# Optimization experiments

Hardware: AMD Instinct MI355X
Metric: run time of the kernel (lower is better)

## Reference

```python
import jax, jax.numpy as jnp
import numpy as np
import math

HEAD = 4
D_MODEL = 128
N_NODES = 2048
SEQ_LEN = 1
D_K = D_MODEL // HEAD
BATCH = 64


def conv1x1_relu(x, w, b):
    # x: [B, C, N, L], w: [O, C], b: [O]  (1x1 Conv2d + ReLU; dropout is identity in eval)
    return jax.nn.relu(jnp.einsum('oc,bcnl->bonl', w, x) + b[None, :, None, None])


def setup_inputs() -> dict:
    key = jax.random.key(0)
    ks = jax.random.split(key, 12)
    s = 0.05
    return {
        'x': jax.random.normal(ks[0], (BATCH, D_MODEL, N_NODES, SEQ_LEN), jnp.float32),
        'q_w': jax.random.normal(ks[1], (D_MODEL, D_MODEL), jnp.float32) * s,
        'q_b': jnp.zeros((D_MODEL,), jnp.float32),
        'v_w': jax.random.normal(ks[2], (D_MODEL, D_MODEL), jnp.float32) * s,
        'v_b': jnp.zeros((D_MODEL,), jnp.float32),
        'c_w': jax.random.normal(ks[3], (D_MODEL, D_MODEL), jnp.float32) * s,
        'c_b': jnp.zeros((D_MODEL,), jnp.float32),
        'memory': jax.random.normal(ks[4], (HEAD, SEQ_LEN, N_NODES, D_K), jnp.float32) * s,
        'nodevec1': jax.random.normal(ks[5], (N_NODES, 10), jnp.float32),
        'nodevec2': jax.random.normal(ks[6], (10, N_NODES), jnp.float32),
        'weights_pool': jax.random.normal(ks[7], (SEQ_LEN, 3, 3), jnp.float32) * s,
        'bias_pool': jax.random.normal(ks[8], (N_NODES, D_K), jnp.float32) * s,
        'aff_w': jnp.ones((D_MODEL, N_NODES, SEQ_LEN), jnp.float32),
        'aff_b': jnp.zeros((D_MODEL, N_NODES, SEQ_LEN), jnp.float32),
    }


def reference(x, q_w, q_b, v_w, v_b, c_w, c_b, memory, nodevec1, nodevec2,
              weights_pool, bias_pool, aff_w, aff_b):
    B = x.shape[0]
    scale = math.sqrt(D_K)

    query = conv1x1_relu(x, q_w, q_b)
    value = conv1x1_relu(x, v_w, v_b)

    # [B, d_model, N, L] -> [B, h, d_k, N, L] -> [B, h, L, N, d_k]
    def split_heads(t):
        return t.reshape(B, HEAD, D_K, N_NODES, SEQ_LEN).transpose(0, 1, 4, 3, 2)

    query = split_heads(query)
    value = split_heads(value)

    key_ = jax.nn.softmax(memory / scale, axis=-1)      # [h, L, N, d_k]
    query = jax.nn.softmax(query / scale, axis=-1)      # [B, h, L, N, d_k]

    Aapt = jax.nn.softmax(jax.nn.relu(nodevec1 @ nodevec2), axis=-1)  # [N, N]

    kv = jnp.einsum('hlnx,bhlny->bhlxy', key_, value)          # [B,h,L,d_k,d_k]
    attn_qkv = jnp.einsum('bhlnx,bhlxy->bhlny', query, kv)     # [B,h,L,N,d_k]

    weights = jnp.einsum('nm,dio->nio', Aapt, weights_pool)    # [N,3,3]
    bias_dyn = Aapt @ bias_pool                                # [N,d_k]
    attn_dyn = jnp.einsum('bhlnc,nio->bhlnc', value, weights) + bias_dyn[None, None, None, :, :]

    out = attn_qkv + attn_dyn                                  # [B,h,L,N,d_k]
    out = out.transpose(0, 1, 4, 3, 2).reshape(B, D_MODEL, N_NODES, SEQ_LEN)
    out = conv1x1_relu(out, c_w, c_b)

    # num_nodes (2048) not in [170, 358, 5] -> affine-residual branch runs
    out = out * aff_w[None] + aff_b[None] + out
    return out
```

## Files before the change

kernel.cpp:

```cpp
#include <hip/hip_runtime.h>

#define NB 64
#define CH 128
#define NNODE 2048
#define NH 4
#define DKK 32
#define INVS 0.17677669529663687f

typedef __bf16 bf16x8 __attribute__((ext_vector_type(8)));
typedef float f32x4 __attribute__((ext_vector_type(4)));
typedef unsigned short ushort_t;

union U16x8 { uint4 u; bf16x8 b; unsigned short s[8]; };
union U16x4 { uint2 u; unsigned short s[4]; };

__device__ inline bf16x8 as_bf16x8(uint4 u){ U16x8 x; x.u = u; return x.b; }
__device__ inline unsigned short f2b(float f){ __bf16 h = (__bf16)f; return __builtin_bit_cast(unsigned short, h); }
__device__ inline float b2f(unsigned short u){ __bf16 h = __builtin_bit_cast(__bf16, u); return (float)h; }

__global__ __launch_bounds__(256) void k0_prep(const float* __restrict__ qw,
    const float* __restrict__ vw, const float* __restrict__ cw,
    const float* __restrict__ memory, const float* __restrict__ bias_pool,
    ushort_t* __restrict__ wqb, ushort_t* __restrict__ wvb, ushort_t* __restrict__ wcb,
    ushort_t* __restrict__ keysT, float* __restrict__ bias_dyn,
    ushort_t* __restrict__ bpT)
{
  int gid = blockIdx.x * 256 + threadIdx.x;
  if (gid < 16384) { wqb[gid] = f2b(qw[gid]); wvb[gid] = f2b(vw[gid]); wcb[gid] = f2b(cw[gid]); }
  bias_dyn[gid] = 0.f;
  { int k = gid >> 11, m = gid & 2047;
    bpT[gid] = f2b(bias_pool[m * 32 + k]); }
  if (gid < 8192) {
    int h = gid >> 11, n = gid & 2047;
    const float* src = memory + (size_t)gid * 32;
    float v[32]; float m = -1e30f;
    #pragma unroll
    for (int i = 0; i < 32; ++i) { v[i] = src[i] * INVS; m = fmaxf(m, v[i]); }
    float s = 0.f;
    #pragma unroll
    for (int i = 0; i < 32; ++i) { v[i] = __expf(v[i] - m); s += v[i]; }
    float inv = 1.f / s;
    #pragma unroll
    for (int i = 0; i < 32; ++i)
      keysT[(size_t)(h * 32 + i) * 2048 + n] = f2b(v[i] * inv);
  }
}

__global__ __launch_bounds__(256) void kb1(const float* __restrict__ nv1,
    const float* __restrict__ nv2, ushort_t* __restrict__ Ebuf)
{
  int n = blockIdx.x; int tid = threadIdx.x;
  float a1[10];
  #pragma unroll
  for (int d = 0; d < 10; ++d) a1[d] = nv1[n * 10 + d];
  int m0 = tid * 8;
  float s[8];
  #pragma unroll
  for (int j = 0; j < 8; ++j) s[j] = 0.f;
  #pragma unroll
  for (int d = 0; d < 10; ++d) {
    const float* p = nv2 + d * 2048 + m0;
    float4 u = *(const float4*)p; float4 v = *(const float4*)(p + 4);
    s[0] += a1[d] * u.x; s[1] += a1[d] * u.y; s[2] += a1[d] * u.z; s[3] += a1[d] * u.w;
    s[4] += a1[d] * v.x; s[5] += a1[d] * v.y; s[6] += a1[d] * v.z; s[7] += a1[d] * v.w;
  }
  float e[8]; float sum = 0.f;
  #pragma unroll
  for (int j = 0; j < 8; ++j) { e[j] = __expf(fmaxf(s[j], 0.f)); sum += e[j]; }
  #pragma unroll
  for (int d = 1; d < 64; d <<= 1) sum += __shfl_xor(sum, d);
  __shared__ float red[4];
  if ((tid & 63) == 0) red[tid >> 6] = sum;
  __syncthreads();
  float inv = 1.f / (red[0] + red[1] + red[2] + red[3]);
  U16x8 o;
  #pragma unroll
  for (int j = 0; j < 8; ++j) o.s[j] = f2b(e[j] * inv);
  *(uint4*)(Ebuf + (size_t)n * 2048 + m0) = o.u;
}

__global__ __launch_bounds__(256) void kb2(const ushort_t* __restrict__ Ebuf,
    const ushort_t* __restrict__ bpT, float* __restrict__ bias_dyn)
{
  int bid = blockIdx.x;
  int n0 = (bid >> 3) * 128;
  int m0 = (bid & 7) * 256;
  int tid = threadIdx.x; int wv = tid >> 6; int lane = tid & 63;
  int quad = lane >> 4; int l16 = lane & 15;
  int r0 = n0 + 32 * wv;
  f32x4 zero4 = {0.f,0.f,0.f,0.f};
  f32x4 acc[2][2];
  acc[0][0] = zero4; acc[0][1] = zero4; acc[1][0] = zero4; acc[1][1] = zero4;
  for (int ks = 0; ks < 256; ks += 32) {
    int mb = m0 + ks + 8 * quad;
    bf16x8 a0 = *(const bf16x8*)(Ebuf + (size_t)(r0 + l16) * 2048 + mb);
    bf16x8 a1 = *(const bf16x8*)(Ebuf + (size_t)(r0 + 16 + l16) * 2048 + mb);
    bf16x8 b0 = *(const bf16x8*)(bpT + (size_t)l16 * 2048 + mb);
    bf16x8 b1 = *(const bf16x8*)(bpT + (size_t)(16 + l16) * 2048 + mb);
    acc[0][0] = __builtin_amdgcn_mfma_f32_16x16x32_bf16(a0, b0, acc[0][0], 0, 0, 0);
    acc[0][1] = __builtin_amdgcn_mfma_f32_16x16x32_bf16(a0, b1, acc[0][1], 0, 0, 0);
    acc[1][0] = __builtin_amdgcn_mfma_f32_16x16x32_bf16(a1, b0, acc[1][0], 0, 0, 0);
    acc[1][1] = __builtin_amdgcn_mfma_f32_16x16x32_bf16(a1, b1, acc[1][1], 0, 0, 0);
  }
  #pragma unroll
  for (int rt = 0; rt < 2; ++rt)
    #pragma unroll
    for (int ct = 0; ct < 2; ++ct)
      #pragma unroll
      for (int r = 0; r < 4; ++r)
        atomicAdd(bias_dyn + (size_t)(r0 + 16*rt + 4*quad + r) * 32 + 16*ct + l16,
                  acc[rt][ct][r]);
}

__global__ __launch_bounds__(256) void k1_qv(const float* __restrict__ x,
    const ushort_t* __restrict__ wqb, const ushort_t* __restrict__ wvb,
    const float* __restrict__ qbias, const float* __restrict__ vbias,
    ushort_t* __restrict__ QsT, ushort_t* __restrict__ VT)
{
  int bid = blockIdx.x; int b = bid >> 5; int n0 = (bid & 31) * 64;
  int tid = threadIdx.x; int wv = tid >> 6; int lane = tid & 63;
  int quad = lane >> 4; int l16 = lane & 15;
  __shared__ __align__(16) ushort_t XT[64][136];
  __shared__ __align__(16) ushort_t QO[64][136];

  uint4 wq[2][4], wvv[2][4];
  #pragma unroll
  for (int ct = 0; ct < 2; ++ct)
    #pragma unroll
    for (int k0 = 0; k0 < 4; ++k0) {
      int off = (32 * wv + 16 * ct + l16) * 128 + 32 * k0 + 8 * quad;
      wq[ct][k0]  = *(const uint4*)(wqb + off);
      wvv[ct][k0] = *(const uint4*)(wvb + off);
    }
  float4 qb4[2], vb4[2];
  #pragma unroll
  for (int ct = 0; ct < 2; ++ct) {
    qb4[ct] = *(const float4*)(qbias + 32 * wv + 16 * ct + 4 * quad);
    vb4[ct] = *(const float4*)(vbias + 32 * wv + 16 * ct + 4 * quad);
  }

  #pragma unroll
  for (int p = 0; p < 2; ++p) {
    int c4 = 4 * ((tid >> 4) + 16 * p);
    int n4 = 4 * (tid & 15);
    float4 r[4];
    #pragma unroll
    for (int j = 0; j < 4; ++j)
      r[j] = *(const float4*)(x + (size_t)(b * 128 + c4 + j) * 2048 + n0 + n4);
    #pragma unroll
    for (int i = 0; i < 4; ++i) {
      U16x4 w;
      w.s[0] = f2b(((const float*)&r[0])[i]);
      w.s[1] = f2b(((const float*)&r[1])[i]);
      w.s[2] = f2b(((const float*)&r[2])[i]);
      w.s[3] = f2b(((const float*)&r[3])[i]);
      *(uint2*)&XT[n4 + i][c4] = w.u;
    }
  }
  __syncthreads();

  f32x4 zero4 = {0.f,0.f,0.f,0.f};
  f32x4 av[4][2];

  #pragma unroll
  for (int nt = 0; nt < 4; ++nt) {
    f32x4 aq[2]; aq[0] = zero4; aq[1] = zero4;
    f32x4 avv[2]; avv[0] = zero4; avv[1] = zero4;
    #pragma unroll
    for (int k0 = 0; k0 < 4; ++k0) {
      bf16x8 bfrag = *(const bf16x8*)&XT[16 * nt + l16][32 * k0 + 8 * quad];
      #pragma unroll
      for (int ct = 0; ct < 2; ++ct) {
        aq[ct]  = __builtin_amdgcn_mfma_f32_16x16x32_bf16(as_bf16x8(wq[ct][k0]),  bfrag, aq[ct],  0, 0, 0);
        avv[ct] = __builtin_amdgcn_mfma_f32_16x16x32_bf16(as_bf16x8(wvv[ct][k0]), bfrag, avv[ct], 0, 0, 0);
      }
    }
    float sq[2][4]; float mx = -1e30f;
    #pragma unroll
    for (int ct = 0; ct < 2; ++ct)
      #pragma unroll
      for (int r = 0; r < 4; ++r) {
        sq[ct][r] = fmaxf(aq[ct][r] + ((const float*)&qb4[ct])[r], 0.f) * INVS;
        mx = fmaxf(mx, sq[ct][r]);
      }
    mx = fmaxf(mx, __shfl_xor(mx, 16));
    mx = fmaxf(mx, __shfl_xor(mx, 32));
    float sum = 0.f;
    #pragma unroll
    for (int ct = 0; ct < 2; ++ct)
      #pragma unroll
      for (int r = 0; r < 4; ++r) { sq[ct][r] = __expf(sq[ct][r] - mx); sum += sq[ct][r]; }
    sum += __shfl_xor(sum, 16);
    sum += __shfl_xor(sum, 32);
    float inv = 1.f / sum;
    #pragma unroll
    for (int ct = 0; ct < 2; ++ct) {
      U16x4 w;
      #pragma unroll
      for (int r = 0; r < 4; ++r) w.s[r] = f2b(sq[ct][r] * inv);
      *(uint2*)&QO[16 * nt + l16][32 * wv + 16 * ct + 4 * quad] = w.u;
    }
    av[nt][0] = avv[0]; av[nt][1] = avv[1];
  }
  __syncthreads();

  #pragma unroll
  for (int nt = 0; nt < 4; ++nt)
    #pragma unroll
    for (int ct = 0; ct < 2; ++ct) {
      U16x4 w;
      #pragma unroll
      for (int r = 0; r < 4; ++r)
        w.s[r] = f2b(fmaxf(av[nt][ct][r] + ((const float*)&vb4[ct])[r], 0.f));
      *(uint2*)&XT[16 * nt + l16][32 * wv + 16 * ct + 4 * quad] = w.u;
    }
  __syncthreads();

  #pragma unroll
  for (int j = 0; j < 4; ++j) {
    int id = tid + 256 * j; int n = id >> 4; int u = id & 15;
    size_t go = (size_t)(b * 2048 + n0 + n) * 128 + 8 * u;
    *(uint4*)(QsT + go) = *(uint4*)&QO[n][8 * u];
    *(uint4*)(VT  + go) = *(uint4*)&XT[n][8 * u];
  }
}

__global__ __launch_bounds__(256) void k2_kv(const ushort_t* __restrict__ keysT,
    const ushort_t* __restrict__ VT, float* __restrict__ kvp)
{
  int bid = blockIdx.x; int b = bid >> 3; int nb = (bid & 7) * 256;
  int tid = threadIdx.x; int wv = tid >> 6; int lane = tid & 63;
  int quad = lane >> 4; int l16 = lane & 15;
  __shared__ __align__(16) ushort_t Vraw[128][136];

  f32x4 zero4 = {0.f,0.f,0.f,0.f};
  f32x4 acc[2][2];
  acc[0][0] = zero4; acc[0][1] = zero4; acc[1][0] = zero4; acc[1][1] = zero4;

  for (int chunk = 0; chunk < 2; ++chunk) {
    int nc = nb + 128 * chunk;
    if (chunk) __syncthreads();
    #pragma unroll
    for (int p = 0; p < 8; ++p) {
      int id = tid + 256 * p; int n = id >> 4; int g = id & 15;
      *(uint4*)&Vraw[n][8 * g] = *(const uint4*)(VT + (size_t)(b * 2048 + nc + n) * 128 + 8 * g);
    }
    __syncthreads();
    const ushort_t* kT = keysT + (size_t)(wv * 32) * 2048 + nc;
    #pragma unroll
    for (int ks = 0; ks < 4; ++ks) {
      int k0 = 32 * ks + 8 * quad;
      bf16x8 a0 = *(const bf16x8*)(kT + (size_t)l16 * 2048 + k0);
      bf16x8 a1 = *(const bf16x8*)(kT + (size_t)(16 + l16) * 2048 + k0);
      U16x8 b0, b1;
      #pragma unroll
      for (int j = 0; j < 8; ++j) {
        b0.s[j] = Vraw[k0 + j][32 * wv + l16];
        b1.s[j] = Vraw[k0 + j][32 * wv + 16 + l16];
      }
      acc[0][0] = __builtin_amdgcn_mfma_f32_16x16x32_bf16(a0, b0.b, acc[0][0], 0, 0, 0);
      acc[0][1] = __builtin_amdgcn_mfma_f32_16x16x32_bf16(a0, b1.b, acc[0][1], 0, 0, 0);
      acc[1][0] = __builtin_amdgcn_mfma_f32_16x16x32_bf16(a1, b0.b, acc[1][0], 0, 0, 0);
      acc[1][1] = __builtin_amdgcn_mfma_f32_16x16x32_bf16(a1, b1.b, acc[1][1], 0, 0, 0);
    }
  }

  float* dst = kvp + (size_t)bid * 4096 + wv * 1024;
  #pragma unroll
  for (int yt = 0; yt < 2; ++yt)
    #pragma unroll
    for (int xt = 0; xt < 2; ++xt)
      #pragma unroll
      for (int r = 0; r < 4; ++r)
        dst[(16 * yt + l16) * 32 + 16 * xt + 4 * quad + r] = acc[xt][yt][r];
}

__global__ __launch_bounds__(256) void kred(const float* __restrict__ kvp,
    float* __restrict__ kvws)
{
  int gid = blockIdx.x * 256 + threadIdx.x;
  int b = gid >> 12; int i = gid & 4095;
  const float* p = kvp + (size_t)(b * 8) * 4096 + i;
  float s = 0.f;
  #pragma unroll
  for (int t = 0; t < 8; ++t) s += p[t * 4096];
  kvws[gid] = s;
}

__global__ __launch_bounds__(256) void k3_out(const ushort_t* __restrict__ QsT,
    const ushort_t* __restrict__ VT, const float* __restrict__ kvws,
    const float* __restrict__ bias_dyn, const ushort_t* __restrict__ wcb,
    const float* __restrict__ cbias, const float* __restrict__ wpool,
    const float* __restrict__ aff_w, const float* __restrict__ aff_b,
    float* __restrict__ out)
{
  int bid = blockIdx.x; int b = bid >> 5; int n0 = (bid & 31) * 64;
  int tid = threadIdx.x; int wv = tid >> 6; int lane = tid & 63;
  int quad = lane >> 4; int l16 = lane & 15;
  __shared__ __align__(16) ushort_t kvT[4][32][40];
  __shared__ __align__(16) ushort_t MID[64][136];
  __shared__ __align__(16) ushort_t VL[64][132];
  __shared__ __align__(16) float    BD[64][36];

  float Ws = 0.f;
  #pragma unroll
  for (int i = 0; i < 9; ++i) Ws += wpool[i];

  uint4 wc[2][4];
  #pragma unroll
  for (int mt = 0; mt < 2; ++mt)
    #pragma unroll
    for (int k0 = 0; k0 < 4; ++k0)
      wc[mt][k0] = *(const uint4*)(wcb + (32 * wv + 16 * mt + l16) * 128 + 32 * k0 + 8 * quad);

  #pragma unroll
  for (int p = 0; p < 16; ++p) {
    int id = tid + 256 * p;
    kvT[id >> 10][(id >> 5) & 31][id & 31] = f2b(kvws[(size_t)b * 4096 + id]);
  }
  #pragma unroll
  for (int p = 0; p < 4; ++p) {
    int id = tid + 256 * p; int n = id >> 4; int u = id & 15;
    *(uint4*)&VL[n][8 * u] = *(const uint4*)(VT + (size_t)(b * 2048 + n0 + n) * 128 + 8 * u);
  }
  #pragma unroll
  for (int p = 0; p < 2; ++p) {
    int id = tid + 256 * p; int n = id >> 3; int g = id & 7;
    *(float4*)&BD[n][4 * g] = *(const float4*)(bias_dyn + (size_t)(n0 + n) * 32 + 4 * g);
  }
  __syncthreads();

  f32x4 zero4 = {0.f,0.f,0.f,0.f};
  f32x4 acc1[4][2];
  #pragma unroll
  for (int nt = 0; nt < 4; ++nt) { acc1[nt][0] = zero4; acc1[nt][1] = zero4; }
  #pragma unroll
  for (int nt = 0; nt < 4; ++nt) {
    bf16x8 aq = *(const bf16x8*)(QsT + (size_t)(b * 2048 + n0 + 16 * nt + l16) * 128 + 32 * wv + 8 * quad);
    #pragma unroll
    for (int ct = 0; ct < 2; ++ct)
      acc1[nt][ct] = __builtin_amdgcn_mfma_f32_16x16x32_bf16(
          aq, *(const bf16x8*)&kvT[wv][16 * ct + l16][8 * quad], acc1[nt][ct], 0, 0, 0);
  }

  #pragma unroll
  for (int nt = 0; nt < 4; ++nt)
    #pragma unroll
    for (int ct = 0; ct < 2; ++ct)
      #pragma unroll
      for (int r = 0; r < 4; ++r) {
        int nl = 16 * nt + 4 * quad + r;
        int cc = 32 * wv + 16 * ct + l16;
        float v = b2f(VL[nl][cc]);
        float bd = BD[nl][16 * ct + l16];
        MID[nl][cc] = f2b(acc1[nt][ct][r] + Ws * v + bd);
      }
  __syncthreads();

  f32x4 acc2[2][4];
  #pragma unroll
  for (int mt = 0; mt < 2; ++mt)
    #pragma unroll
    for (int nt = 0; nt < 4; ++nt) acc2[mt][nt] = zero4;
  #pragma unroll
  for (int k0 = 0; k0 < 4; ++k0) {
    bf16x8 bb[4];
    #pragma unroll
    for (int nt = 0; nt < 4; ++nt)
      bb[nt] = *(const bf16x8*)&MID[16 * nt + l16][32 * k0 + 8 * quad];
    #pragma unroll
    for (int mt = 0; mt < 2; ++mt)
      #pragma unroll
      for (int nt = 0; nt < 4; ++nt)
        acc2[mt][nt] = __builtin_amdgcn_mfma_f32_16x16x32_bf16(
            as_bf16x8(wc[mt][k0]), bb[nt], acc2[mt][nt], 0, 0, 0);
  }

  #pragma unroll
  for (int mt = 0; mt < 2; ++mt)
    #pragma unroll
    for (int nt = 0; nt < 4; ++nt)
      #pragma unroll
      for (int r = 0; r < 4; ++r) {
        int c_out = 32 * wv + 16 * mt + 4 * quad + r;
        int nn2 = n0 + 16 * nt + l16;
        float yv = fmaxf(acc2[mt][nt][r] + cbias[c_out], 0.f);
        size_t ai = (size_t)c_out * 2048 + nn2;
        float awv = aff_w[ai], abv = aff_b[ai];
        out[(size_t)(b * 128 + c_out) * 2048 + nn2] = yv * awv + abv + yv;
      }
}

extern "C" void kernel_launch(void* const* d_in, const int* in_sizes, int n_in,
                              void* d_out, int out_size, void* d_ws, size_t ws_size,
                              hipStream_t stream)
{
  const float* x      = (const float*)d_in[0];
  const float* qw     = (const float*)d_in[1];
  const float* qb     = (const float*)d_in[2];
  const float* vw     = (const float*)d_in[3];
  const float* vb     = (const float*)d_in[4];
  const float* cw     = (const float*)d_in[5];
  const float* cb     = (const float*)d_in[6];
  const float* memory = (const float*)d_in[7];
  const float* nv1    = (const float*)d_in[8];
  const float* nv2    = (const float*)d_in[9];
  const float* wpool  = (const float*)d_in[10];
  const float* bpool  = (const float*)d_in[11];
  const float* aw     = (const float*)d_in[12];
  const float* ab     = (const float*)d_in[13];
  float* out = (float*)d_out;

  char* ws = (char*)d_ws;
  ushort_t* QsT      = (ushort_t*)(ws);
  ushort_t* VT       = (ushort_t*)(ws + 33554432);
  float*    kvws     = (float*)   (ws + 67108864);
  ushort_t* keysT    = (ushort_t*)(ws + 68157440);
  float*    bias_dyn = (float*)   (ws + 69206016);
  ushort_t* wqb      = (ushort_t*)(ws + 69468160);
  ushort_t* wvb      = (ushort_t*)(ws + 69500928);
  ushort_t* wcb      = (ushort_t*)(ws + 69533696);
  ushort_t* Ebuf     = (ushort_t*)(ws + 69566464);
  ushort_t* bpT      = (ushort_t*)(ws + 77955072);
  float*    kvp      = (float*)Ebuf;

  k0_prep<<<256, 256, 0, stream>>>(qw, vw, cw, memory, bpool, wqb, wvb, wcb,
                                   keysT, bias_dyn, bpT);
  kb1<<<2048, 256, 0, stream>>>(nv1, nv2, Ebuf);
  kb2<<<128, 256, 0, stream>>>(Ebuf, bpT, bias_dyn);
  k1_qv<<<2048, 256, 0, stream>>>(x, wqb, wvb, qb, vb, QsT, VT);
  k2_kv<<<512, 256, 0, stream>>>(keysT, VT, kvp);
  kred<<<1024, 256, 0, stream>>>(kvp, kvws);
  k3_out<<<2048, 256, 0, stream>>>(QsT, VT, kvws, bias_dyn, wcb, cb, wpool, aw, ab, out);
}
```

Measured before the change: 212.6 us.

## Store Q and V in channel-blocked layout, drop LDS staging in k1

Changes the intermediate QsT/VT layout from [b][n][128] to a channel-blocked [b][c/4][n][4] form. k1 can then write each MFMA result fragment straight to global memory, which removes the QO shared buffer and two block barriers. k2 and k3 are updated to read the new layout, with new LDS shapes and index math. The x-load transpose loop also rotates its write order per thread to reduce LDS bank conflicts. The cost is narrower 8-byte global stores and split 8-byte loads in k3.

```diff
diff --git a/kernel.cpp b/kernel.cpp
--- a/kernel.cpp
+++ b/kernel.cpp
@@ -17,6 +17,7 @@
 __device__ inline bf16x8 as_bf16x8(uint4 u){ U16x8 x; x.u = u; return x.b; }
 __device__ inline unsigned short f2b(float f){ __bf16 h = (__bf16)f; return __builtin_bit_cast(unsigned short, h); }
 __device__ inline float b2f(unsigned short u){ __bf16 h = __builtin_bit_cast(__bf16, u); return (float)h; }
+
 
 __global__ __launch_bounds__(256) void k0_prep(const float* __restrict__ qw,
     const float* __restrict__ vw, const float* __restrict__ cw,
@@ -121,7 +122,6 @@
   int tid = threadIdx.x; int wv = tid >> 6; int lane = tid & 63;
   int quad = lane >> 4; int l16 = lane & 15;
   __shared__ __align__(16) ushort_t XT[64][136];
-  __shared__ __align__(16) ushort_t QO[64][136];
 
   uint4 wq[2][4], wvv[2][4];
   #pragma unroll
@@ -141,27 +141,26 @@
 
   #pragma unroll
   for (int p = 0; p < 2; ++p) {
-    int c4 = 4 * ((tid >> 4) + 16 * p);
+    int c4 = 4 * (tid >> 4) + 64 * p;
     int n4 = 4 * (tid & 15);
     float4 r[4];
     #pragma unroll
-    for (int j = 0; j < 4; ++j)
-      r[j] = *(const float4*)(x + (size_t)(b * 128 + c4 + j) * 2048 + n0 + n4);
+    for (int k = 0; k < 4; ++k)
+      r[k] = *(const float4*)(x + (size_t)(b * 128 + c4 + k) * 2048 + n0 + n4);
     #pragma unroll
     for (int i = 0; i < 4; ++i) {
+      int j = (i + tid) & 3;
       U16x4 w;
-      w.s[0] = f2b(((const float*)&r[0])[i]);
-      w.s[1] = f2b(((const float*)&r[1])[i]);
-      w.s[2] = f2b(((const float*)&r[2])[i]);
-      w.s[3] = f2b(((const float*)&r[3])[i]);
-      *(uint2*)&XT[n4 + i][c4] = w.u;
+      w.s[0] = f2b(((const float*)&r[0])[j]);
+      w.s[1] = f2b(((const float*)&r[1])[j]);
+      w.s[2] = f2b(((const float*)&r[2])[j]);
+      w.s[3] = f2b(((const float*)&r[3])[j]);
+      *(uint2*)&XT[n4 + j][c4] = w.u;
     }
   }
   __syncthreads();
 
   f32x4 zero4 = {0.f,0.f,0.f,0.f};
-  f32x4 av[4][2];
-
   #pragma unroll
   for (int nt = 0; nt < 4; ++nt) {
     f32x4 aq[2]; aq[0] = zero4; aq[1] = zero4;
@@ -193,35 +192,19 @@
     sum += __shfl_xor(sum, 16);
     sum += __shfl_xor(sum, 32);
     float inv = 1.f / sum;
+    int nn = n0 + 16 * nt + l16;
     #pragma unroll
     for (int ct = 0; ct < 2; ++ct) {
-      U16x4 w;
-      #pragma unroll
-      for (int r = 0; r < 4; ++r) w.s[r] = f2b(sq[ct][r] * inv);
-      *(uint2*)&QO[16 * nt + l16][32 * wv + 16 * ct + 4 * quad] = w.u;
-    }
-    av[nt][0] = avv[0]; av[nt][1] = avv[1];
-  }
-  __syncthreads();
-
-  #pragma unroll
-  for (int nt = 0; nt < 4; ++nt)
-    #pragma unroll
-    for (int ct = 0; ct < 2; ++ct) {
-      U16x4 w;
-      #pragma unroll
-      for (int r = 0; r < 4; ++r)
-        w.s[r] = f2b(fmaxf(av[nt][ct][r] + ((const float*)&vb4[ct])[r], 0.f));
-      *(uint2*)&XT[16 * nt + l16][32 * wv + 16 * ct + 4 * quad] = w.u;
-    }
-  __syncthreads();
-
-  #pragma unroll
-  for (int j = 0; j < 4; ++j) {
-    int id = tid + 256 * j; int n = id >> 4; int u = id & 15;
-    size_t go = (size_t)(b * 2048 + n0 + n) * 128 + 8 * u;
-    *(uint4*)(QsT + go) = *(uint4*)&QO[n][8 * u];
-    *(uint4*)(VT  + go) = *(uint4*)&XT[n][8 * u];
+      size_t go = ((size_t)(b * 32 + 8 * wv + 4 * ct + quad) * 2048 + nn) * 4;
+      U16x4 wQ, wV;
+      #pragma unroll
+      for (int r = 0; r < 4; ++r) {
+        wQ.s[r] = f2b(sq[ct][r] * inv);
+        wV.s[r] = f2b(fmaxf(avv[ct][r] + ((const float*)&vb4[ct])[r], 0.f));
+      }
+      *(uint2*)(QsT + go) = wQ.u;
+      *(uint2*)(VT  + go) = wV.u;
+    }
   }
 }
 
@@ -231,19 +214,22 @@
   int bid = blockIdx.x; int b = bid >> 3; int nb = (bid & 7) * 256;
   int tid = threadIdx.x; int wv = tid >> 6; int lane = tid & 63;
   int quad = lane >> 4; int l16 = lane & 15;
-  __shared__ __align__(16) ushort_t Vraw[128][136];
+  __shared__ __align__(16) ushort_t Vraw[32][520];
 
   f32x4 zero4 = {0.f,0.f,0.f,0.f};
   f32x4 acc[2][2];
   acc[0][0] = zero4; acc[0][1] = zero4; acc[1][0] = zero4; acc[1][1] = zero4;
+  int o0 = 32 * wv + l16, o1 = o0 + 16;
+  int s0 = (o0 >> 2) * 520 + (o0 & 3), s1 = (o1 >> 2) * 520 + (o1 & 3);
 
   for (int chunk = 0; chunk < 2; ++chunk) {
     int nc = nb + 128 * chunk;
     if (chunk) __syncthreads();
     #pragma unroll
     for (int p = 0; p < 8; ++p) {
-      int id = tid + 256 * p; int n = id >> 4; int g = id & 15;
-      *(uint4*)&Vraw[n][8 * g] = *(const uint4*)(VT + (size_t)(b * 2048 + nc + n) * 128 + 8 * g);
+      int id = tid + 256 * p; int cblk = id >> 6; int nn = 2 * (id & 63);
+      *(uint4*)&Vraw[cblk][nn * 4] =
+          *(const uint4*)(VT + ((size_t)(b * 32 + cblk) * 2048 + nc + nn) * 4);
     }
     __syncthreads();
     const ushort_t* kT = keysT + (size_t)(wv * 32) * 2048 + nc;
@@ -255,8 +241,8 @@
       U16x8 b0, b1;
       #pragma unroll
       for (int j = 0; j < 8; ++j) {
-        b0.s[j] = Vraw[k0 + j][32 * wv + l16];
-        b1.s[j] = Vraw[k0 + j][32 * wv + 16 + l16];
+        b0.s[j] = Vraw[0][s0 + 4 * (k0 + j)];
+        b1.s[j] = Vraw[0][s1 + 4 * (k0 + j)];
       }
       acc[0][0] = __builtin_amdgcn_mfma_f32_16x16x32_bf16(a0, b0.b, acc[0][0], 0, 0, 0);
       acc[0][1] = __builtin_amdgcn_mfma_f32_16x16x32_bf16(a0, b1.b, acc[0][1], 0, 0, 0);
@@ -299,7 +285,7 @@
   int quad = lane >> 4; int l16 = lane & 15;
   __shared__ __align__(16) ushort_t kvT[4][32][40];
   __shared__ __align__(16) ushort_t MID[64][136];
-  __shared__ __align__(16) ushort_t VL[64][132];
+  __shared__ __align__(16) ushort_t VL[32][264];
   __shared__ __align__(16) float    BD[64][36];
 
   float Ws = 0.f;
@@ -320,8 +306,9 @@
   }
   #pragma unroll
   for (int p = 0; p < 4; ++p) {
-    int id = tid + 256 * p; int n = id >> 4; int u = id & 15;
-    *(uint4*)&VL[n][8 * u] = *(const uint4*)(VT + (size_t)(b * 2048 + n0 + n) * 128 + 8 * u);
+    int id = tid + 256 * p; int cblk = id >> 5; int nn = 2 * (id & 31);
+    *(uint4*)&VL[cblk][nn * 4] =
+        *(const uint4*)(VT + ((size_t)(b * 32 + cblk) * 2048 + n0 + nn) * 4);
   }
   #pragma unroll
   for (int p = 0; p < 2; ++p) {
@@ -336,11 +323,14 @@
   for (int nt = 0; nt < 4; ++nt) { acc1[nt][0] = zero4; acc1[nt][1] = zero4; }
   #pragma unroll
   for (int nt = 0; nt < 4; ++nt) {
-    bf16x8 aq = *(const bf16x8*)(QsT + (size_t)(b * 2048 + n0 + 16 * nt + l16) * 128 + 32 * wv + 8 * quad);
+    const ushort_t* qp = QsT + ((size_t)(b * 32 + 8 * wv + 2 * quad) * 2048 + n0 + 16 * nt + l16) * 4;
+    uint2 lo = *(const uint2*)qp;
+    uint2 hi = *(const uint2*)(qp + 8192);
+    U16x8 af; af.u = make_uint4(lo.x, lo.y, hi.x, hi.y);
     #pragma unroll
     for (int ct = 0; ct < 2; ++ct)
       acc1[nt][ct] = __builtin_amdgcn_mfma_f32_16x16x32_bf16(
-          aq, *(const bf16x8*)&kvT[wv][16 * ct + l16][8 * quad], acc1[nt][ct], 0, 0, 0);
+          af.b, *(const bf16x8*)&kvT[wv][16 * ct + l16][8 * quad], acc1[nt][ct], 0, 0, 0);
   }
 
   #pragma unroll
@@ -351,7 +341,7 @@
       for (int r = 0; r < 4; ++r) {
         int nl = 16 * nt + 4 * quad + r;
         int cc = 32 * wv + 16 * ct + l16;
-        float v = b2f(VL[nl][cc]);
+        float v = b2f(VL[cc >> 2][nl * 4 + (cc & 3)]);
         float bd = BD[nl][16 * ct + l16];
         MID[nl][cc] = f2b(acc1[nt][ct][r] + Ws * v + bd);
       }
```

After: 226.8 us. +6.7%, slower.
